# Optimization experiments

Hardware: AMD Instinct MI355X
Metric: run time of the kernel (lower is better)

Reference implementation:

```python
import jax, jax.numpy as jnp
import numpy as np

TEMPERATURE = 8.0  # sqrt(d_k) with d_k = 64


def setup_inputs() -> dict:
    key = jax.random.key(0)
    k1, k2, k3, k4 = jax.random.split(key, 4)
    B, S, D = 16, 2048, 64  # B = batch * n_heads
    q = jax.random.normal(k1, (B, S, D), dtype=jnp.float32)
    k = jax.random.normal(k2, (B, S, D), dtype=jnp.float32)
    v = jax.random.normal(k3, (B, S, D), dtype=jnp.float32)
    # boolean mask: True = masked out. Low prob so no row is fully masked.
    mask = jax.random.uniform(k4, (B, S, S)) < 0.1
    return {"q": q, "k": k, "v": v, "mask": mask}


def reference(q, k, v, mask):
    # attn = (q @ k^T) / temperature, masked_fill(mask, -inf), softmax over last dim
    attn = jnp.einsum("bqd,bkd->bqk", q, k) / TEMPERATURE
    attn = jnp.where(mask, -jnp.inf, attn)
    attn = jax.nn.softmax(attn, axis=2)
    output = jnp.einsum("bqk,bkd->bqd", attn, v)
    return output, attn
```

## Files before the change

### kernel.cpp

```cpp
#include <hip/hip_runtime.h>

typedef _Float16 half8 __attribute__((ext_vector_type(8)));
typedef _Float16 half4 __attribute__((ext_vector_type(4)));
typedef float    floatx4 __attribute__((ext_vector_type(4)));

#define NB  16
#define SEQ 2048
#define DIM 64

#define MFMA32(a,b,c) __builtin_amdgcn_mfma_f32_16x16x32_f16((a),(b),(c),0,0,0)
#define MFMA16(a,b,c) __builtin_amdgcn_mfma_f32_16x16x16f16((a),(b),(c),0,0,0)

__global__ __launch_bounds__(256) void cvt_qk_kernel(const float* __restrict__ q,
                                                     const float* __restrict__ k,
                                                     _Float16* __restrict__ qh,
                                                     _Float16* __restrict__ kh) {
    size_t i = ((size_t)blockIdx.x * 256 + threadIdx.x) * 4;
    float4 a = *(const float4*)(q + i);
    float4 b = *(const float4*)(k + i);
    half4 ha = { (_Float16)a.x, (_Float16)a.y, (_Float16)a.z, (_Float16)a.w };
    half4 hb = { (_Float16)b.x, (_Float16)b.y, (_Float16)b.z, (_Float16)b.w };
    *(half4*)(qh + i) = ha;
    *(half4*)(kh + i) = hb;
}

__global__ __launch_bounds__(256) void cvt_vt_kernel(const float* __restrict__ v,
                                                     _Float16* __restrict__ vt) {
    __shared__ float tile[64][65];
    const int b  = blockIdx.x >> 5;
    const int s0 = (blockIdx.x & 31) << 6;
    const int t  = threadIdx.x;
    {
        const int row = t >> 2;
        const int c0  = (t & 3) << 4;
        const float* src = v + ((size_t)(b * SEQ + s0 + row)) * DIM + c0;
        #pragma unroll
        for (int i = 0; i < 4; ++i) {
            float4 x = *(const float4*)(src + i * 4);
            tile[row][c0 + i*4 + 0] = x.x;
            tile[row][c0 + i*4 + 1] = x.y;
            tile[row][c0 + i*4 + 2] = x.z;
            tile[row][c0 + i*4 + 3] = x.w;
        }
    }
    __syncthreads();
    {
        const int d  = t >> 2;
        const int sb = (t & 3) << 4;
        _Float16* dst = vt + ((size_t)(b * DIM + d)) * SEQ + s0 + sb;
        #pragma unroll
        for (int i = 0; i < 4; ++i) {
            half4 h = { (_Float16)tile[sb + i*4 + 0][d],
                        (_Float16)tile[sb + i*4 + 1][d],
                        (_Float16)tile[sb + i*4 + 2][d],
                        (_Float16)tile[sb + i*4 + 3][d] };
            *(half4*)(dst + i*4) = h;
        }
    }
}

__global__ __launch_bounds__(256) void mask_bits_kernel(const int* __restrict__ mask,
                                                        unsigned int* __restrict__ bits) {
    const int wave = threadIdx.x >> 6;
    const int lane = threadIdx.x & 63;
    const size_t row = (size_t)blockIdx.x * 4 + wave;
    const int* mp = mask + row * SEQ + lane;
    unsigned int keep = 0;
    #pragma unroll
    for (int it = 0; it < 32; ++it) {
        int m = __builtin_nontemporal_load(mp + it * 64);
        unsigned long long bal = __ballot(m != 0);
        unsigned int half = (lane & 1) ? (unsigned int)(bal >> 32) : (unsigned int)bal;
        if ((lane >> 1) == it) keep = half;
    }
    bits[row * 64 + lane] = keep;
}

__global__ __launch_bounds__(256, 6) void attn_kernel(
    const _Float16* __restrict__ qh, const _Float16* __restrict__ kh,
    const _Float16* __restrict__ vt, const unsigned int* __restrict__ bits,
    float* __restrict__ out, float* __restrict__ attn)
{
    __shared__ float wsum[4][16];
    __shared__ __align__(16) float outred[4][16][68];

    const int blk  = ((blockIdx.x & 7) << 8) + (blockIdx.x >> 3);
    const int b    = blk >> 7;
    const int r0   = (blk & 127) << 4;
    const int lane = threadIdx.x & 63;
    const int wave = threadIdx.x >> 6;
    const int rl   = lane & 15;
    const int g    = lane >> 4;

    const size_t qoff = ((size_t)(b * SEQ + r0 + rl)) * DIM + g * 8;
    const half8 qa0 = *(const half8*)(qh + qoff);
    const half8 qa1 = *(const half8*)(qh + qoff + 32);

    const _Float16* kbase = kh + (size_t)b * SEQ * DIM + (size_t)rl * DIM + g * 8;
    const _Float16* vbase = vt + ((size_t)b * DIM + rl) * SEQ + g * 4;
    const unsigned int* bbase = bits + ((size_t)(b * SEQ + r0 + rl)) * 64 + wave;

    float rs = 0.f;
    floatx4 o0 = {0.f,0.f,0.f,0.f}, o1 = {0.f,0.f,0.f,0.f};
    floatx4 o2 = {0.f,0.f,0.f,0.f}, o3 = {0.f,0.f,0.f,0.f};
    unsigned int pb = bbase[0];

    for (int cc = 0; cc < 16; ++cc) {
        const int jj = (cc * 4 + wave) * 32;
        const unsigned int bm = pb;
        if (cc < 15) pb = bbase[(cc + 1) * 4];
        const _Float16* kp = kbase + (size_t)jj * DIM;
        half8 ka0 = *(const half8*)(kp);
        half8 ka1 = *(const half8*)(kp + 32);
        half8 kb0 = *(const half8*)(kp + 16 * DIM);
        half8 kb1 = *(const half8*)(kp + 16 * DIM + 32);
        floatx4 c0 = {0.f,0.f,0.f,0.f}, c1 = {0.f,0.f,0.f,0.f};
        c0 = MFMA32(ka0, qa0, c0);
        c0 = MFMA32(ka1, qa1, c0);
        c1 = MFMA32(kb0, qa0, c1);
        c1 = MFMA32(kb1, qa1, c1);
        const unsigned int blo = bm >> (g * 4);
        const unsigned int bhi = bm >> (g * 4 + 16);
        float e0 = (blo & 1u) ? 0.f : __expf(c0[0] * 0.125f);
        float e1 = (blo & 2u) ? 0.f : __expf(c0[1] * 0.125f);
        float e2 = (blo & 4u) ? 0.f : __expf(c0[2] * 0.125f);
        float e3 = (blo & 8u) ? 0.f : __expf(c0[3] * 0.125f);
        float e4 = (bhi & 1u) ? 0.f : __expf(c1[0] * 0.125f);
        float e5 = (bhi & 2u) ? 0.f : __expf(c1[1] * 0.125f);
        float e6 = (bhi & 4u) ? 0.f : __expf(c1[2] * 0.125f);
        float e7 = (bhi & 8u) ? 0.f : __expf(c1[3] * 0.125f);
        rs += (e0 + e1) + (e2 + e3) + (e4 + e5) + (e6 + e7);

        half4 h0 = { (_Float16)e0, (_Float16)e1, (_Float16)e2, (_Float16)e3 };
        half4 h1 = { (_Float16)e4, (_Float16)e5, (_Float16)e6, (_Float16)e7 };

        const _Float16* vp = vbase + jj;
        half4 va00 = *(const half4*)(vp);
        half4 va01 = *(const half4*)(vp + 16);
        half4 va10 = *(const half4*)(vp + 16 * SEQ);
        half4 va11 = *(const half4*)(vp + 16 * SEQ + 16);
        half4 va20 = *(const half4*)(vp + 32 * SEQ);
        half4 va21 = *(const half4*)(vp + 32 * SEQ + 16);
        half4 va30 = *(const half4*)(vp + 48 * SEQ);
        half4 va31 = *(const half4*)(vp + 48 * SEQ + 16);
        o0 = MFMA16(va00, h0, o0);
        o0 = MFMA16(va01, h1, o0);
        o1 = MFMA16(va10, h0, o1);
        o1 = MFMA16(va11, h1, o1);
        o2 = MFMA16(va20, h0, o2);
        o2 = MFMA16(va21, h1, o2);
        o3 = MFMA16(va30, h0, o3);
        o3 = MFMA16(va31, h1, o3);
    }

    rs += __shfl_xor(rs, 16);
    rs += __shfl_xor(rs, 32);
    if (g == 0) wsum[wave][rl] = rs;
    __syncthreads();
    const float inv = 1.0f / (wsum[0][rl] + wsum[1][rl] + wsum[2][rl] + wsum[3][rl]);

    float* abase = attn + ((size_t)(b * SEQ + r0 + rl)) * SEQ + g * 4;

    for (int cc = 0; cc < 16; ++cc) {
        const int jj = (cc * 4 + wave) * 32;
        const unsigned int bm = bbase[cc * 4];
        const _Float16* kp = kbase + (size_t)jj * DIM;
        half8 ka0 = *(const half8*)(kp);
        half8 ka1 = *(const half8*)(kp + 32);
        half8 kb0 = *(const half8*)(kp + 16 * DIM);
        half8 kb1 = *(const half8*)(kp + 16 * DIM + 32);
        floatx4 c0 = {0.f,0.f,0.f,0.f}, c1 = {0.f,0.f,0.f,0.f};
        c0 = MFMA32(ka0, qa0, c0);
        c0 = MFMA32(ka1, qa1, c0);
        c1 = MFMA32(kb0, qa0, c1);
        c1 = MFMA32(kb1, qa1, c1);

        const unsigned int blo = bm >> (g * 4);
        const unsigned int bhi = bm >> (g * 4 + 16);
        float e0 = (blo & 1u) ? 0.f : __expf(c0[0] * 0.125f);
        float e1 = (blo & 2u) ? 0.f : __expf(c0[1] * 0.125f);
        float e2 = (blo & 4u) ? 0.f : __expf(c0[2] * 0.125f);
        float e3 = (blo & 8u) ? 0.f : __expf(c0[3] * 0.125f);
        float e4 = (bhi & 1u) ? 0.f : __expf(c1[0] * 0.125f);
        float e5 = (bhi & 2u) ? 0.f : __expf(c1[1] * 0.125f);
        float e6 = (bhi & 4u) ? 0.f : __expf(c1[2] * 0.125f);
        float e7 = (bhi & 8u) ? 0.f : __expf(c1[3] * 0.125f);

        floatx4 a0 = { e0 * inv, e1 * inv, e2 * inv, e3 * inv };
        floatx4 a1 = { e4 * inv, e5 * inv, e6 * inv, e7 * inv };
        *(floatx4*)(abase + jj)      = a0;
        *(floatx4*)(abase + jj + 16) = a1;
    }

    {
        float* orow = &outred[wave][rl][g * 4];
        *(floatx4*)(orow +  0) = o0;
        *(floatx4*)(orow + 16) = o1;
        *(floatx4*)(orow + 32) = o2;
        *(floatx4*)(orow + 48) = o3;
    }
    __syncthreads();
    {
        const int r  = threadIdx.x >> 4;
        const int c4 = (threadIdx.x & 15) << 2;
        floatx4 s0 = *(const floatx4*)(&outred[0][r][c4]);
        floatx4 s1 = *(const floatx4*)(&outred[1][r][c4]);
        floatx4 s2 = *(const floatx4*)(&outred[2][r][c4]);
        floatx4 s3 = *(const floatx4*)(&outred[3][r][c4]);
        floatx4 s = (s0 + s1) + (s2 + s3);
        const float inv2 = 1.0f / (wsum[0][r] + wsum[1][r] + wsum[2][r] + wsum[3][r]);
        floatx4 ov = { s[0] * inv2, s[1] * inv2, s[2] * inv2, s[3] * inv2 };
        *(floatx4*)(out + ((size_t)(b * SEQ + r0 + r)) * DIM + c4) = ov;
    }
}

extern "C" void kernel_launch(void* const* d_in, const int* in_sizes, int n_in,
                              void* d_out, int out_size, void* d_ws, size_t ws_size,
                              hipStream_t stream) {
    const float* q = (const float*)d_in[0];
    const float* k = (const float*)d_in[1];
    const float* v = (const float*)d_in[2];
    const int* mask = (const int*)d_in[3];

    float* out  = (float*)d_out;
    float* attn = out + (size_t)NB * SEQ * DIM;

    _Float16* qh = (_Float16*)d_ws;
    _Float16* kh = qh + (size_t)NB * SEQ * DIM;
    _Float16* vt = kh + (size_t)NB * SEQ * DIM;
    unsigned int* bits = (unsigned int*)(vt + (size_t)NB * SEQ * DIM);

    cvt_qk_kernel<<<(NB * SEQ * DIM) / 1024, 256, 0, stream>>>(q, k, qh, kh);
    cvt_vt_kernel<<<NB * (SEQ / 64), 256, 0, stream>>>(v, vt);
    mask_bits_kernel<<<(NB * SEQ) / 4, 256, 0, stream>>>(mask, bits);
    attn_kernel<<<NB * (SEQ / 16), 256, 0, stream>>>(qh, kh, vt, bits, out, attn);
}
```

Baseline: 667.1 us.

## Move PV accumulation into second pass and unroll first pass and mask loads

The first pass now computes only the row sums, unrolled two chunks at a time for more memory-level parallelism. The P·V MFMA accumulation moves into the second pass, which already recomputes the exponentials to write the attention matrix, so that work overlaps with the large attn stores. The mask-bit kernel issues all 32 loads before the ballots, and the XCD-aware block swizzle is dropped in favour of linear block indexing. The risks are higher register pressure in the second loop, which could hurt occupancy, and worse L2 locality for K and V without the swizzle.

```diff
diff --git a/kernel.cpp b/kernel.cpp
--- a/kernel.cpp
+++ b/kernel.cpp
@@ -65,11 +65,14 @@
     const int lane = threadIdx.x & 63;
     const size_t row = (size_t)blockIdx.x * 4 + wave;
     const int* mp = mask + row * SEQ + lane;
+    int m[32];
+    #pragma unroll
+    for (int it = 0; it < 32; ++it)
+        m[it] = __builtin_nontemporal_load(mp + it * 64);
     unsigned int keep = 0;
     #pragma unroll
     for (int it = 0; it < 32; ++it) {
-        int m = __builtin_nontemporal_load(mp + it * 64);
-        unsigned long long bal = __ballot(m != 0);
+        unsigned long long bal = __ballot(m[it] != 0);
         unsigned int half = (lane & 1) ? (unsigned int)(bal >> 32) : (unsigned int)bal;
         if ((lane >> 1) == it) keep = half;
     }
@@ -84,9 +87,8 @@
     __shared__ float wsum[4][16];
     __shared__ __align__(16) float outred[4][16][68];
 
-    const int blk  = ((blockIdx.x & 7) << 8) + (blockIdx.x >> 3);
-    const int b    = blk >> 7;
-    const int r0   = (blk & 127) << 4;
+    const int b    = blockIdx.x >> 7;
+    const int r0   = (blockIdx.x & 127) << 4;
     const int lane = threadIdx.x & 63;
     const int wave = threadIdx.x >> 6;
     const int rl   = lane & 15;
@@ -101,24 +103,92 @@
     const unsigned int* bbase = bits + ((size_t)(b * SEQ + r0 + rl)) * 64 + wave;
 
     float rs = 0.f;
+
+    for (int cc = 0; cc < 16; cc += 2) {
+        const int jA = ((cc    ) * 4 + wave) * 32;
+        const int jB = ((cc + 1) * 4 + wave) * 32;
+        const unsigned int bmA = bbase[cc * 4];
+        const unsigned int bmB = bbase[cc * 4 + 4];
+        const _Float16* kpA = kbase + (size_t)jA * DIM;
+        const _Float16* kpB = kbase + (size_t)jB * DIM;
+        half8 ka0 = *(const half8*)(kpA);
+        half8 ka1 = *(const half8*)(kpA + 32);
+        half8 ka2 = *(const half8*)(kpA + 16 * DIM);
+        half8 ka3 = *(const half8*)(kpA + 16 * DIM + 32);
+        half8 kb0 = *(const half8*)(kpB);
+        half8 kb1 = *(const half8*)(kpB + 32);
+        half8 kb2 = *(const half8*)(kpB + 16 * DIM);
+        half8 kb3 = *(const half8*)(kpB + 16 * DIM + 32);
+
+        floatx4 cA0 = {0.f,0.f,0.f,0.f}, cA1 = {0.f,0.f,0.f,0.f};
+        floatx4 cB0 = {0.f,0.f,0.f,0.f}, cB1 = {0.f,0.f,0.f,0.f};
+        cA0 = MFMA32(ka0, qa0, cA0);
+        cA0 = MFMA32(ka1, qa1, cA0);
+        cA1 = MFMA32(ka2, qa0, cA1);
+        cA1 = MFMA32(ka3, qa1, cA1);
+        cB0 = MFMA32(kb0, qa0, cB0);
+        cB0 = MFMA32(kb1, qa1, cB0);
+        cB1 = MFMA32(kb2, qa0, cB1);
+        cB1 = MFMA32(kb3, qa1, cB1);
+
+        const unsigned int aLo = bmA >> (g * 4);
+        const unsigned int aHi = bmA >> (g * 4 + 16);
+        const unsigned int bLo = bmB >> (g * 4);
+        const unsigned int bHi = bmB >> (g * 4 + 16);
+        float e0 = (aLo & 1u) ? 0.f : __expf(cA0[0] * 0.125f);
+        float e1 = (aLo & 2u) ? 0.f : __expf(cA0[1] * 0.125f);
+        float e2 = (aLo & 4u) ? 0.f : __expf(cA0[2] * 0.125f);
+        float e3 = (aLo & 8u) ? 0.f : __expf(cA0[3] * 0.125f);
+        float e4 = (aHi & 1u) ? 0.f : __expf(cA1[0] * 0.125f);
+        float e5 = (aHi & 2u) ? 0.f : __expf(cA1[1] * 0.125f);
+        float e6 = (aHi & 4u) ? 0.f : __expf(cA1[2] * 0.125f);
+        float e7 = (aHi & 8u) ? 0.f : __expf(cA1[3] * 0.125f);
+        float f0 = (bLo & 1u) ? 0.f : __expf(cB0[0] * 0.125f);
+        float f1 = (bLo & 2u) ? 0.f : __expf(cB0[1] * 0.125f);
+        float f2 = (bLo & 4u) ? 0.f : __expf(cB0[2] * 0.125f);
+        float f3 = (bLo & 8u) ? 0.f : __expf(cB0[3] * 0.125f);
+        float f4 = (bHi & 1u) ? 0.f : __expf(cB1[0] * 0.125f);
+        float f5 = (bHi & 2u) ? 0.f : __expf(cB1[1] * 0.125f);
+        float f6 = (bHi & 4u) ? 0.f : __expf(cB1[2] * 0.125f);
+        float f7 = (bHi & 8u) ? 0.f : __expf(cB1[3] * 0.125f);
+        rs += ((e0 + e1) + (e2 + e3)) + ((e4 + e5) + (e6 + e7))
+            + ((f0 + f1) + (f2 + f3)) + ((f4 + f5) + (f6 + f7));
+    }
+
+    rs += __shfl_xor(rs, 16);
+    rs += __shfl_xor(rs, 32);
+    if (g == 0) wsum[wave][rl] = rs;
+    __syncthreads();
+    const float inv = 1.0f / (wsum[0][rl] + wsum[1][rl] + wsum[2][rl] + wsum[3][rl]);
+
     floatx4 o0 = {0.f,0.f,0.f,0.f}, o1 = {0.f,0.f,0.f,0.f};
     floatx4 o2 = {0.f,0.f,0.f,0.f}, o3 = {0.f,0.f,0.f,0.f};
-    unsigned int pb = bbase[0];
+    float* abase = attn + ((size_t)(b * SEQ + r0 + rl)) * SEQ + g * 4;
 
     for (int cc = 0; cc < 16; ++cc) {
         const int jj = (cc * 4 + wave) * 32;
-        const unsigned int bm = pb;
-        if (cc < 15) pb = bbase[(cc + 1) * 4];
+        const unsigned int bm = bbase[cc * 4];
         const _Float16* kp = kbase + (size_t)jj * DIM;
         half8 ka0 = *(const half8*)(kp);
         half8 ka1 = *(const half8*)(kp + 32);
         half8 kb0 = *(const half8*)(kp + 16 * DIM);
         half8 kb1 = *(const half8*)(kp + 16 * DIM + 32);
+        const _Float16* vp = vbase + jj;
+        half4 va00 = *(const half4*)(vp);
+        half4 va01 = *(const half4*)(vp + 16);
+        half4 va10 = *(const half4*)(vp + 16 * SEQ);
+        half4 va11 = *(const half4*)(vp + 16 * SEQ + 16);
+        half4 va20 = *(const half4*)(vp + 32 * SEQ);
+        half4 va21 = *(const half4*)(vp + 32 * SEQ + 16);
+        half4 va30 = *(const half4*)(vp + 48 * SEQ);
+        half4 va31 = *(const half4*)(vp + 48 * SEQ + 16);
+
         floatx4 c0 = {0.f,0.f,0.f,0.f}, c1 = {0.f,0.f,0.f,0.f};
         c0 = MFMA32(ka0, qa0, c0);
         c0 = MFMA32(ka1, qa1, c0);
         c1 = MFMA32(kb0, qa0, c1);
         c1 = MFMA32(kb1, qa1, c1);
+
         const unsigned int blo = bm >> (g * 4);
         const unsigned int bhi = bm >> (g * 4 + 16);
         float e0 = (blo & 1u) ? 0.f : __expf(c0[0] * 0.125f);
@@ -129,20 +199,9 @@
         float e5 = (bhi & 2u) ? 0.f : __expf(c1[1] * 0.125f);
         float e6 = (bhi & 4u) ? 0.f : __expf(c1[2] * 0.125f);
         float e7 = (bhi & 8u) ? 0.f : __expf(c1[3] * 0.125f);
-        rs += (e0 + e1) + (e2 + e3) + (e4 + e5) + (e6 + e7);
 
         half4 h0 = { (_Float16)e0, (_Float16)e1, (_Float16)e2, (_Float16)e3 };
         half4 h1 = { (_Float16)e4, (_Float16)e5, (_Float16)e6, (_Float16)e7 };
-
-        const _Float16* vp = vbase + jj;
-        half4 va00 = *(const half4*)(vp);
-        half4 va01 = *(const half4*)(vp + 16);
-        half4 va10 = *(const half4*)(vp + 16 * SEQ);
-        half4 va11 = *(const half4*)(vp + 16 * SEQ + 16);
-        half4 va20 = *(const half4*)(vp + 32 * SEQ);
-        half4 va21 = *(const half4*)(vp + 32 * SEQ + 16);
-        half4 va30 = *(const half4*)(vp + 48 * SEQ);
-        half4 va31 = *(const half4*)(vp + 48 * SEQ + 16);
         o0 = MFMA16(va00, h0, o0);
         o0 = MFMA16(va01, h1, o0);
         o1 = MFMA16(va10, h0, o1);
@@ -151,40 +210,6 @@
         o2 = MFMA16(va21, h1, o2);
         o3 = MFMA16(va30, h0, o3);
         o3 = MFMA16(va31, h1, o3);
-    }
-
-    rs += __shfl_xor(rs, 16);
-    rs += __shfl_xor(rs, 32);
-    if (g == 0) wsum[wave][rl] = rs;
-    __syncthreads();
-    const float inv = 1.0f / (wsum[0][rl] + wsum[1][rl] + wsum[2][rl] + wsum[3][rl]);
-
-    float* abase = attn + ((size_t)(b * SEQ + r0 + rl)) * SEQ + g * 4;
-
-    for (int cc = 0; cc < 16; ++cc) {
-        const int jj = (cc * 4 + wave) * 32;
-        const unsigned int bm = bbase[cc * 4];
-        const _Float16* kp = kbase + (size_t)jj * DIM;
-        half8 ka0 = *(const half8*)(kp);
-        half8 ka1 = *(const half8*)(kp + 32);
-        half8 kb0 = *(const half8*)(kp + 16 * DIM);
-        half8 kb1 = *(const half8*)(kp + 16 * DIM + 32);
-        floatx4 c0 = {0.f,0.f,0.f,0.f}, c1 = {0.f,0.f,0.f,0.f};
-        c0 = MFMA32(ka0, qa0, c0);
-        c0 = MFMA32(ka1, qa1, c0);
-        c1 = MFMA32(kb0, qa0, c1);
-        c1 = MFMA32(kb1, qa1, c1);
-
-        const unsigned int blo = bm >> (g * 4);
-        const unsigned int bhi = bm >> (g * 4 + 16);
-        float e0 = (blo & 1u) ? 0.f : __expf(c0[0] * 0.125f);
-        float e1 = (blo & 2u) ? 0.f : __expf(c0[1] * 0.125f);
-        float e2 = (blo & 4u) ? 0.f : __expf(c0[2] * 0.125f);
-        float e3 = (blo & 8u) ? 0.f : __expf(c0[3] * 0.125f);
-        float e4 = (bhi & 1u) ? 0.f : __expf(c1[0] * 0.125f);
-        float e5 = (bhi & 2u) ? 0.f : __expf(c1[1] * 0.125f);
-        float e6 = (bhi & 4u) ? 0.f : __expf(c1[2] * 0.125f);
-        float e7 = (bhi & 8u) ? 0.f : __expf(c1[3] * 0.125f);
 
         floatx4 a0 = { e0 * inv, e1 * inv, e2 * inv, e3 * inv };
         floatx4 a1 = { e4 * inv, e5 * inv, e6 * inv, e7 * inv };
```

Result: no change. 666.9 us (-0.0%).
